# Performance work log

Hardware: AMD Instinct MI355X
Metric: run time of the kernel (lower is better)

## Reference

```python
import math
import jax, jax.numpy as jnp
import numpy as np

NUM_HEADS = 16
QUERY_SIZE = 1024
SEQ = 2048
HEAD = QUERY_SIZE // NUM_HEADS  # qk_size = vo_size = 64


def setup_inputs() -> dict:
    key = jax.random.key(0)
    ks = jax.random.split(key, 8)
    s = 0.02
    query = jax.random.normal(ks[0], (SEQ, QUERY_SIZE), jnp.float32)
    key_ = jax.random.normal(ks[1], (SEQ, QUERY_SIZE), jnp.float32)
    value = jax.random.normal(ks[2], (SEQ, QUERY_SIZE), jnp.float32)
    # causal mask (mask='causal' with state=None -> offset 0)
    mask = jnp.tril(jnp.ones((SEQ, SEQ), dtype=bool))
    Wq = jax.random.normal(ks[3], (QUERY_SIZE, QUERY_SIZE), jnp.float32) * s
    Wk = jax.random.normal(ks[4], (QUERY_SIZE, QUERY_SIZE), jnp.float32) * s
    Wv = jax.random.normal(ks[5], (QUERY_SIZE, QUERY_SIZE), jnp.float32) * s
    Wo = jax.random.normal(ks[6], (QUERY_SIZE, QUERY_SIZE), jnp.float32) * s
    return {"query": query, "key_": key_, "value": value, "mask": mask,
            "Wq": Wq, "Wk": Wk, "Wv": Wv, "Wo": Wo}


def reference(query, key_, value, mask, Wq, Wk, Wv, Wo):
    H, D = NUMS = NUM_HEADS, HEAD
    S = query.shape[0]
    inv_sqrt_d = 1.0 / math.sqrt(D)
    # per-token linear projections, split into heads: [S, H, D]
    q = (query @ Wq.T).reshape(S, H, D)
    k = (key_ @ Wk.T).reshape(S, H, D)
    v = (value @ Wv.T).reshape(S, H, D)
    # NOTE: original divides BOTH q and k by sqrt(d) (effective 1/d scaling)
    q = q * inv_sqrt_d
    k = k * inv_sqrt_d
    # logits per head: [H, S, S]
    logits = jnp.einsum('shd,Shd->hsS', q, k)
    logits = jnp.where(mask[None, :, :], logits, jnp.finfo(logits.dtype).min)
    # per-head GLOBAL max subtraction, softmax in fp32, cast back (faithful)
    m = jnp.max(logits, axis=(1, 2), keepdims=True)
    weights = jax.nn.softmax((logits - m).astype(jnp.float32), axis=-1).astype(query.dtype)
    attn = jnp.einsum('hsS,ShD->shD', weights, v).reshape(S, H * D)
    return attn @ Wo.T
```

## Files before the change

kernel.cpp:

```cpp
#include <hip/hip_runtime.h>
#include <hip/hip_bf16.h>

typedef __bf16 bf16_t;
typedef __bf16 bf16x8 __attribute__((ext_vector_type(8)));
typedef float f32x4 __attribute__((ext_vector_type(4)));

#define MFMA(A, B, C) __builtin_amdgcn_mfma_f32_16x16x32_bf16(A, B, C, 0, 0, 0)

#define GLL16(g, l) __builtin_amdgcn_global_load_lds(                      \
    (const __attribute__((address_space(1))) void*)(g),                    \
    (__attribute__((address_space(3))) void*)(l), 16, 0, 0)

__global__ __launch_bounds__(256) void cvt_all(
    const float* __restrict__ q, const float* __restrict__ k, const float* __restrict__ v,
    const float* __restrict__ wq, const float* __restrict__ wk,
    const float* __restrict__ wv, const float* __restrict__ wo,
    bf16_t* __restrict__ xq, bf16_t* __restrict__ xk, bf16_t* __restrict__ xv,
    bf16_t* __restrict__ ywq, bf16_t* __restrict__ ywk,
    bf16_t* __restrict__ ywv, bf16_t* __restrict__ ywo)
{
  const long gid = (long)blockIdx.x * 256 + threadIdx.x;
  const float* s; bf16_t* d; long off; float sc = 1.0f;
  if (gid < 262144)       { s = q;  d = xq;  off = gid; }
  else if (gid < 524288)  { s = k;  d = xk;  off = gid - 262144; }
  else if (gid < 786432)  { s = v;  d = xv;  off = gid - 524288; }
  else if (gid < 917504)  { s = wq; d = ywq; off = gid - 786432;  sc = 0.125f; }
  else if (gid < 1048576) { s = wk; d = ywk; off = gid - 917504;  sc = 0.125f; }
  else if (gid < 1179648) { s = wv; d = ywv; off = gid - 1048576; }
  else                    { s = wo; d = ywo; off = gid - 1179648; }
  const float* p = s + off * 8;
  float4 a = *(const float4*)p, b = *(const float4*)(p + 4);
  bf16x8 o;
  o[0] = (bf16_t)(a.x * sc); o[1] = (bf16_t)(a.y * sc);
  o[2] = (bf16_t)(a.z * sc); o[3] = (bf16_t)(a.w * sc);
  o[4] = (bf16_t)(b.x * sc); o[5] = (bf16_t)(b.y * sc);
  o[6] = (bf16_t)(b.z * sc); o[7] = (bf16_t)(b.w * sc);
  *(bf16x8*)(d + off * 8) = o;
}

__device__ __forceinline__ void gemm_core(const bf16_t* __restrict__ A,
                                          const bf16_t* __restrict__ W,
                                          int bm, int bn,
                                          bf16_t (&As)[2][128 * 64],
                                          bf16_t (&Bs)[2][64 * 64],
                                          f32x4 (&acc)[4][2])
{
  const int tid = threadIdx.x, lane = tid & 63, wave = tid >> 6;
  const int l15 = lane & 15, l4 = lane >> 4, l7 = l15 & 7;
  const int wm = (wave >> 1) * 64, wn = (wave & 1) * 32;

  auto stage = [&](int buf, int k0) {
#pragma unroll
    for (int i = 0; i < 4; ++i) {
      const int id = i * 256 + tid, row = id >> 3, cph = id & 7;
      GLL16(A + (size_t)(bm + row) * 1024 + k0 + 8 * (cph ^ (row & 7)),
            &As[buf][(i * 256 + wave * 64) * 8]);
    }
#pragma unroll
    for (int i = 0; i < 2; ++i) {
      const int id = i * 256 + tid, row = id >> 3, cph = id & 7;
      GLL16(W + (size_t)(bn + row) * 1024 + k0 + 8 * (cph ^ (row & 7)),
            &Bs[buf][(i * 256 + wave * 64) * 8]);
    }
  };

  stage(0, 0);
#pragma unroll
  for (int s = 0; s < 16; ++s) {
    if (s + 1 < 16) stage((s + 1) & 1, (s + 1) * 64);
    __syncthreads();
    const bf16_t* as = As[s & 1];
    const bf16_t* bs = Bs[s & 1];
#pragma unroll
    for (int ks = 0; ks < 2; ++ks) {
      bf16x8 af[4], bfr[2];
#pragma unroll
      for (int i = 0; i < 4; ++i)
        af[i] = *(const bf16x8*)(&as[(wm + i * 16 + l15) * 64 + 8 * ((ks * 4 + l4) ^ l7)]);
#pragma unroll
      for (int j = 0; j < 2; ++j)
        bfr[j] = *(const bf16x8*)(&bs[(wn + j * 16 + l15) * 64 + 8 * ((ks * 4 + l4) ^ l7)]);
#pragma unroll
      for (int i = 0; i < 4; ++i)
#pragma unroll
        for (int j = 0; j < 2; ++j)
          acc[i][j] = MFMA(af[i], bfr[j], acc[i][j]);
    }
    __syncthreads();
  }
}

__global__ __launch_bounds__(256) void gemm_qkv(
    const bf16_t* __restrict__ xq, const bf16_t* __restrict__ xk, const bf16_t* __restrict__ xv,
    const bf16_t* __restrict__ ywq, const bf16_t* __restrict__ ywk, const bf16_t* __restrict__ ywv,
    bf16_t* __restrict__ qo, bf16_t* __restrict__ ko, bf16_t* __restrict__ vt)
{
  __shared__ __align__(16) bf16_t As[2][128 * 64];
  __shared__ __align__(16) bf16_t Bs[2][64 * 64];
  const int z = blockIdx.z;
  const bf16_t* A = z == 0 ? xq : z == 1 ? xk : xv;
  const bf16_t* W = z == 0 ? ywq : z == 1 ? ywk : ywv;
  const int bm = blockIdx.x * 128, bn = blockIdx.y * 64;
  f32x4 acc[4][2] = {};
  gemm_core(A, W, bm, bn, As, Bs, acc);
  const int tid = threadIdx.x, lane = tid & 63, wave = tid >> 6;
  const int l15 = lane & 15, l4 = lane >> 4;
  const int wm = (wave >> 1) * 64, wn = (wave & 1) * 32;
  if (z < 2) {
    bf16_t* C = z == 0 ? qo : ko;
#pragma unroll
    for (int i = 0; i < 4; ++i)
#pragma unroll
      for (int j = 0; j < 2; ++j)
#pragma unroll
        for (int r = 0; r < 4; ++r)
          C[(size_t)(bm + wm + i * 16 + 4 * l4 + r) * 1024 + bn + wn + j * 16 + l15] =
              (bf16_t)acc[i][j][r];
  } else {
#pragma unroll
    for (int i = 0; i < 4; ++i)
#pragma unroll
      for (int j = 0; j < 2; ++j)
#pragma unroll
        for (int r = 0; r < 4; ++r)
          vt[(size_t)(bn + wn + j * 16 + l15) * 2048 + bm + wm + i * 16 + 4 * l4 + r] =
              (bf16_t)acc[i][j][r];
  }
}

__global__ __launch_bounds__(256) void gemm_out(
    const bf16_t* __restrict__ ctx, const bf16_t* __restrict__ ywo, float* __restrict__ out)
{
  __shared__ __align__(16) bf16_t As[2][128 * 64];
  __shared__ __align__(16) bf16_t Bs[2][64 * 64];
  const int bm = blockIdx.x * 128, bn = blockIdx.y * 64;
  f32x4 acc[4][2] = {};
  gemm_core(ctx, ywo, bm, bn, As, Bs, acc);
  const int tid = threadIdx.x, lane = tid & 63, wave = tid >> 6;
  const int l15 = lane & 15, l4 = lane >> 4;
  const int wm = (wave >> 1) * 64, wn = (wave & 1) * 32;
#pragma unroll
  for (int i = 0; i < 4; ++i)
#pragma unroll
    for (int j = 0; j < 2; ++j)
#pragma unroll
      for (int r = 0; r < 4; ++r)
        out[(size_t)(bm + wm + i * 16 + 4 * l4 + r) * 1024 + bn + wn + j * 16 + l15] =
            acc[i][j][r];
}

__global__ __launch_bounds__(1024) void attn1024(
    const bf16_t* __restrict__ Qb, const bf16_t* __restrict__ Kb,
    const bf16_t* __restrict__ Vt, bf16_t* __restrict__ Ctx)
{
  __shared__ __align__(16) char pool[64 * 1024 + 16 * 16 * 40 * 2 + 3 * 64 * 4];
  bf16_t* KsP = (bf16_t*)pool;
  bf16_t* VsP = (bf16_t*)(pool + 32 * 1024);
  bf16_t* PsP = (bf16_t*)(pool + 64 * 1024);
  float*  Osc = (float*)pool;
  float*  Dsc = (float*)(pool + 64 * 1024 + 16 * 16 * 40 * 2);

  const int bid = blockIdx.x;
  const int h = 2 * (bid & 7) + (bid >> 7);
  const int jp = (bid >> 3) & 15;
  const int hoff = h * 64;
  const int tid = threadIdx.x, lane = tid & 63, wave = tid >> 6;
  const int qg = wave & 3, kh = wave >> 2;
  const int l15 = lane & 15, l4 = lane >> 4, l7 = l15 & 7;

  const int qtA = jp, qtB = 31 - jp;
  const int qbA = qtA * 64, qbB = qtB * 64;
  const int nscB = qtB / 2 + 1;
  const int qmaxA = qbA + 16 * qg + 15;
  const int qmaxB = qbB + 16 * qg + 15;

  bf16x8 qA[2], qB[2];
#pragma unroll
  for (int kc = 0; kc < 2; ++kc) {
    qA[kc] = *(const bf16x8*)(Qb + (size_t)(qbA + 16 * qg + l15) * 1024 + hoff + 32 * kc + 8 * l4);
    qB[kc] = *(const bf16x8*)(Qb + (size_t)(qbB + 16 * qg + l15) * 1024 + hoff + 32 * kc + 8 * l4);
  }

  f32x4 oA[4] = {}, oB[4] = {};
  float dA[4] = {0.f, 0.f, 0.f, 0.f}, dB[4] = {0.f, 0.f, 0.f, 0.f};

  bf16x8 rk, rv;
  auto issue = [&](int sc) {
    const int t0 = sc * 128;
    const int kr = tid >> 3, kc = tid & 7;
    rk = *(const bf16x8*)(Kb + (size_t)(t0 + kr) * 1024 + hoff + 8 * kc);
    const int vr = tid >> 4, vc = tid & 15;
    rv = *(const bf16x8*)(Vt + (size_t)(hoff + vr) * 2048 + t0 + 8 * vc);
  };
  auto commit = [&](int buf) {
    const int kr = tid >> 3, kc = tid & 7;
    *(bf16x8*)(&KsP[buf * 8192 + kr * 64 + 8 * (kc ^ (kr & 7))]) = rk;
    const int vr = tid >> 4, vc = tid & 15;
    *(bf16x8*)(&VsP[buf * 8192 + vr * 128 + 8 * (vc ^ (vr & 7))]) = rv;
  };

  bf16_t* Pw = &PsP[wave * 640];
  auto PROC1 = [&](int cur, int sc, int qb, int qmax, const bf16x8 (&qf)[2],
                   f32x4 (&oacc)[4], float (&den)[4]) {
    const int tb = sc * 128 + kh * 32;
    if (tb > qmax) return;
    const bf16_t* Ksb = KsP + cur * 8192;
    const bf16_t* Vsb = VsP + cur * 8192;
    f32x4 sv[2] = {};
#pragma unroll
    for (int tf = 0; tf < 2; ++tf) {
      const int krow = 32 * kh + 16 * tf + l15;
      bf16x8 kf0 = *(const bf16x8*)(&Ksb[krow * 64 + 8 * (l4 ^ l7)]);
      bf16x8 kf1 = *(const bf16x8*)(&Ksb[krow * 64 + 8 * ((4 + l4) ^ l7)]);
      sv[tf] = MFMA(qf[0], kf0, sv[tf]);
      sv[tf] = MFMA(qf[1], kf1, sv[tf]);
    }
#pragma unroll
    for (int tf = 0; tf < 2; ++tf) {
      const int t = tb + 16 * tf + l15;
#pragma unroll
      for (int r = 0; r < 4; ++r) {
        const int qq = qb + 16 * qg + 4 * l4 + r;
        const float p = (t <= qq) ? __expf(sv[tf][r]) : 0.0f;
        const bf16_t pb = (bf16_t)p;
        den[r] += (float)pb;
        Pw[(4 * l4 + r) * 40 + 16 * tf + l15] = pb;
      }
    }
    asm volatile("s_waitcnt lgkmcnt(0)" ::: "memory");
    bf16x8 pa = *(const bf16x8*)(&Pw[l15 * 40 + 8 * l4]);
#pragma unroll
    for (int df = 0; df < 4; ++df) {
      const int vrow = 16 * df + l15;
      bf16x8 vf = *(const bf16x8*)(&Vsb[vrow * 128 + 8 * ((4 * kh + l4) ^ l7)]);
      oacc[df] = MFMA(pa, vf, oacc[df]);
    }
  };

  issue(0);
  commit(0);
  int cur = 0;
  for (int sc = 0; sc < nscB; ++sc) {
    const bool pre = (sc + 1 < nscB);
    if (pre) issue(sc + 1);
    __syncthreads();
    PROC1(cur, sc, qbB, qmaxB, qB, oB, dB);
    PROC1(cur, sc, qbA, qmaxA, qA, oA, dA);
    if (pre) commit(cur ^ 1);
    cur ^= 1;
  }

#pragma unroll
  for (int r = 0; r < 4; ++r)
#pragma unroll
    for (int m = 1; m < 16; m <<= 1) {
      dA[r] += __shfl_xor(dA[r], m, 64);
      dB[r] += __shfl_xor(dB[r], m, 64);
    }

  auto combine = [&](int qb, f32x4 (&oacc)[4], float (&den)[4]) {
    __syncthreads();
    if (kh > 0) {
      const int rl = qg * 16 + 4 * l4;
#pragma unroll
      for (int r = 0; r < 4; ++r) {
#pragma unroll
        for (int df = 0; df < 4; ++df)
          Osc[((kh - 1) * 64 + rl + r) * 66 + 16 * df + l15] = oacc[df][r];
        if (l15 == 0) Dsc[(kh - 1) * 64 + rl + r] = den[r];
      }
    }
    __syncthreads();
    if (kh == 0) {
#pragma unroll
      for (int r = 0; r < 4; ++r) {
        const int row = qg * 16 + 4 * l4 + r;
        const float dt = den[r] + Dsc[row] + Dsc[64 + row] + Dsc[128 + row];
        const float inv = 1.0f / dt;
#pragma unroll
        for (int df = 0; df < 4; ++df) {
          const int col = 16 * df + l15;
          const float s = oacc[df][r] + Osc[row * 66 + col] +
                          Osc[(64 + row) * 66 + col] + Osc[(128 + row) * 66 + col];
          Ctx[(size_t)(qb + row) * 1024 + hoff + col] = (bf16_t)(s * inv);
        }
      }
    }
  };
  combine(qbA, oA, dA);
  combine(qbB, oB, dB);
}

extern "C" void kernel_launch(void* const* d_in, const int* in_sizes, int n_in,
                              void* d_out, int out_size, void* d_ws, size_t ws_size,
                              hipStream_t stream)
{
  const float* query = (const float*)d_in[0];
  const float* key_  = (const float*)d_in[1];
  const float* value = (const float*)d_in[2];
  const float* Wq = (const float*)d_in[4];
  const float* Wk = (const float*)d_in[5];
  const float* Wv = (const float*)d_in[6];
  const float* Wo = (const float*)d_in[7];
  float* out = (float*)d_out;

  const size_t SE = (size_t)2048 * 1024, EE = (size_t)1024 * 1024;
  bf16_t* xq  = (bf16_t*)d_ws;
  bf16_t* xk  = xq + SE;
  bf16_t* xv  = xk + SE;
  bf16_t* wq  = xv + SE;
  bf16_t* wk  = wq + EE;
  bf16_t* wv  = wk + EE;
  bf16_t* wo  = wv + EE;
  bf16_t* qo  = wo + EE;
  bf16_t* ko  = qo + SE;
  bf16_t* vt  = ko + SE;
  bf16_t* ctx = vt + SE;

  cvt_all<<<5120, 256, 0, stream>>>(query, key_, value, Wq, Wk, Wv, Wo,
                                    xq, xk, xv, wq, wk, wv, wo);
  gemm_qkv<<<dim3(16, 16, 3), 256, 0, stream>>>(xq, xk, xv, wq, wk, wv, qo, ko, vt);
  attn1024<<<256, 1024, 0, stream>>>(qo, ko, vt, ctx);
  gemm_out<<<dim3(16, 16), 256, 0, stream>>>(ctx, wo, out);
}
```

Before: 71.54 us.

## Split attention into one 512-thread block per query tile with exp2 and mask specialization

Replaces the paired-tile 1024-thread attention kernel with a 512-thread kernel that handles one 64-row query tile per block, two key halves per 64-key chunk, launched heaviest tiles first across 512 blocks. Folds log2(e) into the Wk bf16 conversion so the softmax can use the hardware exp2 directly. Adds a compile-time unmasked path for chunks fully below the diagonal and accumulates the denominator from fp32 rather than rounded bf16 values. The aim is better occupancy and load balance and less per-element work, at the cost of more blocks and a denominator that no longer matches the bf16-rounded weights exactly.

Result: slower. 75.58 us (+5.6%).

```diff
diff --git a/kernel.cpp b/kernel.cpp
--- a/kernel.cpp
+++ b/kernel.cpp
@@ -25,7 +25,7 @@
   else if (gid < 524288)  { s = k;  d = xk;  off = gid - 262144; }
   else if (gid < 786432)  { s = v;  d = xv;  off = gid - 524288; }
   else if (gid < 917504)  { s = wq; d = ywq; off = gid - 786432;  sc = 0.125f; }
-  else if (gid < 1048576) { s = wk; d = ywk; off = gid - 917504;  sc = 0.125f; }
+  else if (gid < 1048576) { s = wk; d = ywk; off = gid - 917504;  sc = 0.125f * 1.44269504f; }
   else if (gid < 1179648) { s = wv; d = ywv; off = gid - 1048576; }
   else                    { s = wo; d = ywo; off = gid - 1179648; }
   const float* p = s + off * 8;
@@ -149,63 +149,56 @@
             acc[i][j][r];
 }
 
-__global__ __launch_bounds__(1024) void attn1024(
+__global__ __launch_bounds__(512) void attn512v2(
     const bf16_t* __restrict__ Qb, const bf16_t* __restrict__ Kb,
     const bf16_t* __restrict__ Vt, bf16_t* __restrict__ Ctx)
 {
-  __shared__ __align__(16) char pool[64 * 1024 + 16 * 16 * 40 * 2 + 3 * 64 * 4];
+  __shared__ __align__(16) char pool[16384 + 16384 + 10240 + 256];
   bf16_t* KsP = (bf16_t*)pool;
-  bf16_t* VsP = (bf16_t*)(pool + 32 * 1024);
-  bf16_t* PsP = (bf16_t*)(pool + 64 * 1024);
+  bf16_t* VsP = (bf16_t*)(pool + 16384);
+  bf16_t* PsP = (bf16_t*)(pool + 32768);
   float*  Osc = (float*)pool;
-  float*  Dsc = (float*)(pool + 64 * 1024 + 16 * 16 * 40 * 2);
+  float*  Dsc = (float*)(pool + 43008);
 
   const int bid = blockIdx.x;
-  const int h = 2 * (bid & 7) + (bid >> 7);
-  const int jp = (bid >> 3) & 15;
+  const int qt = 31 - (bid >> 4);
+  const int h = bid & 15;
   const int hoff = h * 64;
   const int tid = threadIdx.x, lane = tid & 63, wave = tid >> 6;
   const int qg = wave & 3, kh = wave >> 2;
   const int l15 = lane & 15, l4 = lane >> 4, l7 = l15 & 7;
 
-  const int qtA = jp, qtB = 31 - jp;
-  const int qbA = qtA * 64, qbB = qtB * 64;
-  const int nscB = qtB / 2 + 1;
-  const int qmaxA = qbA + 16 * qg + 15;
-  const int qmaxB = qbB + 16 * qg + 15;
-
-  bf16x8 qA[2], qB[2];
-#pragma unroll
-  for (int kc = 0; kc < 2; ++kc) {
-    qA[kc] = *(const bf16x8*)(Qb + (size_t)(qbA + 16 * qg + l15) * 1024 + hoff + 32 * kc + 8 * l4);
-    qB[kc] = *(const bf16x8*)(Qb + (size_t)(qbB + 16 * qg + l15) * 1024 + hoff + 32 * kc + 8 * l4);
-  }
-
-  f32x4 oA[4] = {}, oB[4] = {};
-  float dA[4] = {0.f, 0.f, 0.f, 0.f}, dB[4] = {0.f, 0.f, 0.f, 0.f};
+  const int qb = qt * 64;
+  const int nch = qt + 1;
+  const int qmin = qb + 16 * qg;
+
+  bf16x8 qf[2];
+#pragma unroll
+  for (int kc = 0; kc < 2; ++kc)
+    qf[kc] = *(const bf16x8*)(Qb + (size_t)(qb + 16 * qg + l15) * 1024 + hoff + 32 * kc + 8 * l4);
+
+  f32x4 oacc[4] = {};
+  float den[4] = {0.f, 0.f, 0.f, 0.f};
 
   bf16x8 rk, rv;
-  auto issue = [&](int sc) {
-    const int t0 = sc * 128;
+  auto issue = [&](int c) {
+    const int t0 = c * 64;
     const int kr = tid >> 3, kc = tid & 7;
     rk = *(const bf16x8*)(Kb + (size_t)(t0 + kr) * 1024 + hoff + 8 * kc);
-    const int vr = tid >> 4, vc = tid & 15;
-    rv = *(const bf16x8*)(Vt + (size_t)(hoff + vr) * 2048 + t0 + 8 * vc);
+    rv = *(const bf16x8*)(Vt + (size_t)(hoff + kr) * 2048 + t0 + 8 * kc);
   };
   auto commit = [&](int buf) {
     const int kr = tid >> 3, kc = tid & 7;
-    *(bf16x8*)(&KsP[buf * 8192 + kr * 64 + 8 * (kc ^ (kr & 7))]) = rk;
-    const int vr = tid >> 4, vc = tid & 15;
-    *(bf16x8*)(&VsP[buf * 8192 + vr * 128 + 8 * (vc ^ (vr & 7))]) = rv;
+    *(bf16x8*)(&KsP[buf * 4096 + kr * 64 + 8 * (kc ^ (kr & 7))]) = rk;
+    *(bf16x8*)(&VsP[buf * 4096 + kr * 64 + 8 * (kc ^ (kr & 7))]) = rv;
   };
 
   bf16_t* Pw = &PsP[wave * 640];
-  auto PROC1 = [&](int cur, int sc, int qb, int qmax, const bf16x8 (&qf)[2],
-                   f32x4 (&oacc)[4], float (&den)[4]) {
-    const int tb = sc * 128 + kh * 32;
-    if (tb > qmax) return;
-    const bf16_t* Ksb = KsP + cur * 8192;
-    const bf16_t* Vsb = VsP + cur * 8192;
+  auto PROC = [&](int cur, int c, auto masked) {
+    const int tb = c * 64 + kh * 32;
+    if (tb > qmin + 15) return;
+    const bf16_t* Ksb = KsP + cur * 4096;
+    const bf16_t* Vsb = VsP + cur * 4096;
     f32x4 sv[2] = {};
 #pragma unroll
     for (int tf = 0; tf < 2; ++tf) {
@@ -220,11 +213,13 @@
       const int t = tb + 16 * tf + l15;
 #pragma unroll
       for (int r = 0; r < 4; ++r) {
-        const int qq = qb + 16 * qg + 4 * l4 + r;
-        const float p = (t <= qq) ? __expf(sv[tf][r]) : 0.0f;
-        const bf16_t pb = (bf16_t)p;
-        den[r] += (float)pb;
-        Pw[(4 * l4 + r) * 40 + 16 * tf + l15] = pb;
+        float p = __builtin_amdgcn_exp2f(sv[tf][r]);
+        if constexpr (decltype(masked)::value) {
+          const int qq = qb + 16 * qg + 4 * l4 + r;
+          p = (t <= qq) ? p : 0.0f;
+        }
+        den[r] += p;
+        Pw[(4 * l4 + r) * 40 + 16 * tf + l15] = (bf16_t)p;
       }
     }
     asm volatile("s_waitcnt lgkmcnt(0)" ::: "memory");
@@ -232,7 +227,7 @@
 #pragma unroll
     for (int df = 0; df < 4; ++df) {
       const int vrow = 16 * df + l15;
-      bf16x8 vf = *(const bf16x8*)(&Vsb[vrow * 128 + 8 * ((4 * kh + l4) ^ l7)]);
+      bf16x8 vf = *(const bf16x8*)(&Vsb[vrow * 64 + 8 * ((4 * kh + l4) ^ l7)]);
       oacc[df] = MFMA(pa, vf, oacc[df]);
     }
   };
@@ -240,12 +235,15 @@
   issue(0);
   commit(0);
   int cur = 0;
-  for (int sc = 0; sc < nscB; ++sc) {
-    const bool pre = (sc + 1 < nscB);
-    if (pre) issue(sc + 1);
+  for (int c = 0; c < nch; ++c) {
+    const bool pre = (c + 1 < nch);
+    if (pre) issue(c + 1);
     __syncthreads();
-    PROC1(cur, sc, qbB, qmaxB, qB, oB, dB);
-    PROC1(cur, sc, qbA, qmaxA, qA, oA, dA);
+    const int tb = c * 64 + kh * 32;
+    if (tb + 31 <= qmin)
+      PROC(cur, c, std::integral_constant<bool, false>{});
+    else
+      PROC(cur, c, std::integral_constant<bool, true>{});
     if (pre) commit(cur ^ 1);
     cur ^= 1;
   }
@@ -253,42 +251,34 @@
 #pragma unroll
   for (int r = 0; r < 4; ++r)
 #pragma unroll
-    for (int m = 1; m < 16; m <<= 1) {
-      dA[r] += __shfl_xor(dA[r], m, 64);
-      dB[r] += __shfl_xor(dB[r], m, 64);
-    }
-
-  auto combine = [&](int qb, f32x4 (&oacc)[4], float (&den)[4]) {
-    __syncthreads();
-    if (kh > 0) {
-      const int rl = qg * 16 + 4 * l4;
-#pragma unroll
-      for (int r = 0; r < 4; ++r) {
-#pragma unroll
-        for (int df = 0; df < 4; ++df)
-          Osc[((kh - 1) * 64 + rl + r) * 66 + 16 * df + l15] = oacc[df][r];
-        if (l15 == 0) Dsc[(kh - 1) * 64 + rl + r] = den[r];
+    for (int m = 1; m < 16; m <<= 1)
+      den[r] += __shfl_xor(den[r], m, 64);
+
+  __syncthreads();
+  if (kh == 1) {
+    const int rl = qg * 16 + 4 * l4;
+#pragma unroll
+    for (int r = 0; r < 4; ++r) {
+#pragma unroll
+      for (int df = 0; df < 4; ++df)
+        Osc[(rl + r) * 66 + 16 * df + l15] = oacc[df][r];
+      if (l15 == 0) Dsc[rl + r] = den[r];
+    }
+  }
+  __syncthreads();
+  if (kh == 0) {
+#pragma unroll
+    for (int r = 0; r < 4; ++r) {
+      const int row = qg * 16 + 4 * l4 + r;
+      const float inv = 1.0f / (den[r] + Dsc[row]);
+#pragma unroll
+      for (int df = 0; df < 4; ++df) {
+        const int col = 16 * df + l15;
+        const float s = oacc[df][r] + Osc[row * 66 + col];
+        Ctx[(size_t)(qb + row) * 1024 + hoff + col] = (bf16_t)(s * inv);
       }
     }
-    __syncthreads();
-    if (kh == 0) {
-#pragma unroll
-      for (int r = 0; r < 4; ++r) {
-        const int row = qg * 16 + 4 * l4 + r;
-        const float dt = den[r] + Dsc[row] + Dsc[64 + row] + Dsc[128 + row];
-        const float inv = 1.0f / dt;
-#pragma unroll
-        for (int df = 0; df < 4; ++df) {
-          const int col = 16 * df + l15;
-          const float s = oacc[df][r] + Osc[row * 66 + col] +
-                          Osc[(64 + row) * 66 + col] + Osc[(128 + row) * 66 + col];
-          Ctx[(size_t)(qb + row) * 1024 + hoff + col] = (bf16_t)(s * inv);
-        }
-      }
-    }
-  };
-  combine(qbA, oA, dA);
-  combine(qbB, oB, dB);
+  }
 }
 
 extern "C" void kernel_launch(void* const* d_in, const int* in_sizes, int n_in,
@@ -320,6 +310,6 @@
   cvt_all<<<5120, 256, 0, stream>>>(query, key_, value, Wq, Wk, Wv, Wo,
                                     xq, xk, xv, wq, wk, wv, wo);
   gemm_qkv<<<dim3(16, 16, 3), 256, 0, stream>>>(xq, xk, xv, wq, wk, wv, qo, ko, vt);
-  attn1024<<<256, 1024, 0, stream>>>(qo, ko, vt, ctx);
+  attn512v2<<<512, 512, 0, stream>>>(qo, ko, vt, ctx);
   gemm_out<<<dim3(16, 16), 256, 0, stream>>>(ctx, wo, out);
 }
```

## Double KV chunk size, share K fragments across both query tiles, use exp2

Applied to the files above, without the earlier changes.

The K/V chunk staged per iteration grows from 128 to 256 keys, which halves the number of block barriers and doubles the LDS buffers. Processing of the two paired query tiles is merged, so each K fragment read from LDS feeds the MFMAs for both tiles. The log2(e) factor is folded into the Wk conversion scale so the softmax can use the hardware exp2 instruction instead of __expf. The cost is much more shared memory (about 148KB) and more registers, which could limit occupancy. The coarser chunks also do more masked work near the causal diagonal.

Measured after the change: 79.05 us. 10.5% more time.

```diff
diff --git a/kernel.cpp b/kernel.cpp
--- a/kernel.cpp
+++ b/kernel.cpp
@@ -25,7 +25,7 @@
   else if (gid < 524288)  { s = k;  d = xk;  off = gid - 262144; }
   else if (gid < 786432)  { s = v;  d = xv;  off = gid - 524288; }
   else if (gid < 917504)  { s = wq; d = ywq; off = gid - 786432;  sc = 0.125f; }
-  else if (gid < 1048576) { s = wk; d = ywk; off = gid - 917504;  sc = 0.125f; }
+  else if (gid < 1048576) { s = wk; d = ywk; off = gid - 917504;  sc = 0.125f * 1.44269504f; }
   else if (gid < 1179648) { s = wv; d = ywv; off = gid - 1048576; }
   else                    { s = wo; d = ywo; off = gid - 1179648; }
   const float* p = s + off * 8;
@@ -153,12 +153,12 @@
     const bf16_t* __restrict__ Qb, const bf16_t* __restrict__ Kb,
     const bf16_t* __restrict__ Vt, bf16_t* __restrict__ Ctx)
 {
-  __shared__ __align__(16) char pool[64 * 1024 + 16 * 16 * 40 * 2 + 3 * 64 * 4];
+  __shared__ __align__(16) char pool[64 * 1024 + 64 * 1024 + 16 * 640 * 2];
   bf16_t* KsP = (bf16_t*)pool;
-  bf16_t* VsP = (bf16_t*)(pool + 32 * 1024);
-  bf16_t* PsP = (bf16_t*)(pool + 64 * 1024);
+  bf16_t* VsP = (bf16_t*)(pool + 65536);
+  bf16_t* PsP = (bf16_t*)(pool + 131072);
   float*  Osc = (float*)pool;
-  float*  Dsc = (float*)(pool + 64 * 1024 + 16 * 16 * 40 * 2);
+  float*  Dsc = (float*)(pool + 50688);
 
   const int bid = blockIdx.x;
   const int h = 2 * (bid & 7) + (bid >> 7);
@@ -170,7 +170,7 @@
 
   const int qtA = jp, qtB = 31 - jp;
   const int qbA = qtA * 64, qbB = qtB * 64;
-  const int nscB = qtB / 2 + 1;
+  const int nscB = qtB / 4 + 1;
   const int qmaxA = qbA + 16 * qg + 15;
   const int qmaxB = qbB + 16 * qg + 15;
 
@@ -184,56 +184,95 @@
   f32x4 oA[4] = {}, oB[4] = {};
   float dA[4] = {0.f, 0.f, 0.f, 0.f}, dB[4] = {0.f, 0.f, 0.f, 0.f};
 
-  bf16x8 rk, rv;
+  bf16x8 rk[2], rv[2];
   auto issue = [&](int sc) {
-    const int t0 = sc * 128;
-    const int kr = tid >> 3, kc = tid & 7;
-    rk = *(const bf16x8*)(Kb + (size_t)(t0 + kr) * 1024 + hoff + 8 * kc);
-    const int vr = tid >> 4, vc = tid & 15;
-    rv = *(const bf16x8*)(Vt + (size_t)(hoff + vr) * 2048 + t0 + 8 * vc);
+    const int t0 = sc * 256;
+#pragma unroll
+    for (int i = 0; i < 2; ++i) {
+      const int id = tid + 1024 * i;
+      const int kr = id >> 3, kc = id & 7;
+      rk[i] = *(const bf16x8*)(Kb + (size_t)(t0 + kr) * 1024 + hoff + 8 * kc);
+      const int vr = id >> 5, vc = id & 31;
+      rv[i] = *(const bf16x8*)(Vt + (size_t)(hoff + vr) * 2048 + t0 + 8 * vc);
+    }
   };
   auto commit = [&](int buf) {
-    const int kr = tid >> 3, kc = tid & 7;
-    *(bf16x8*)(&KsP[buf * 8192 + kr * 64 + 8 * (kc ^ (kr & 7))]) = rk;
-    const int vr = tid >> 4, vc = tid & 15;
-    *(bf16x8*)(&VsP[buf * 8192 + vr * 128 + 8 * (vc ^ (vr & 7))]) = rv;
+#pragma unroll
+    for (int i = 0; i < 2; ++i) {
+      const int id = tid + 1024 * i;
+      const int kr = id >> 3, kc = id & 7;
+      *(bf16x8*)(&KsP[buf * 16384 + kr * 64 + 8 * (kc ^ (kr & 7))]) = rk[i];
+      const int vr = id >> 5, vc = id & 31;
+      *(bf16x8*)(&VsP[buf * 16384 + vr * 256 + 8 * (vc ^ (vr & 7))]) = rv[i];
+    }
   };
 
   bf16_t* Pw = &PsP[wave * 640];
-  auto PROC1 = [&](int cur, int sc, int qb, int qmax, const bf16x8 (&qf)[2],
-                   f32x4 (&oacc)[4], float (&den)[4]) {
-    const int tb = sc * 128 + kh * 32;
-    if (tb > qmax) return;
-    const bf16_t* Ksb = KsP + cur * 8192;
-    const bf16_t* Vsb = VsP + cur * 8192;
-    f32x4 sv[2] = {};
-#pragma unroll
-    for (int tf = 0; tf < 2; ++tf) {
-      const int krow = 32 * kh + 16 * tf + l15;
-      bf16x8 kf0 = *(const bf16x8*)(&Ksb[krow * 64 + 8 * (l4 ^ l7)]);
-      bf16x8 kf1 = *(const bf16x8*)(&Ksb[krow * 64 + 8 * ((4 + l4) ^ l7)]);
-      sv[tf] = MFMA(qf[0], kf0, sv[tf]);
-      sv[tf] = MFMA(qf[1], kf1, sv[tf]);
-    }
-#pragma unroll
-    for (int tf = 0; tf < 2; ++tf) {
-      const int t = tb + 16 * tf + l15;
-#pragma unroll
-      for (int r = 0; r < 4; ++r) {
-        const int qq = qb + 16 * qg + 4 * l4 + r;
-        const float p = (t <= qq) ? __expf(sv[tf][r]) : 0.0f;
-        const bf16_t pb = (bf16_t)p;
-        den[r] += (float)pb;
-        Pw[(4 * l4 + r) * 40 + 16 * tf + l15] = pb;
-      }
-    }
-    asm volatile("s_waitcnt lgkmcnt(0)" ::: "memory");
-    bf16x8 pa = *(const bf16x8*)(&Pw[l15 * 40 + 8 * l4]);
-#pragma unroll
-    for (int df = 0; df < 4; ++df) {
-      const int vrow = 16 * df + l15;
-      bf16x8 vf = *(const bf16x8*)(&Vsb[vrow * 128 + 8 * ((4 * kh + l4) ^ l7)]);
-      oacc[df] = MFMA(pa, vf, oacc[df]);
+  auto PROC = [&](int cur, int sc) {
+    const bf16_t* Ksb = KsP + cur * 16384;
+    const bf16_t* Vsb = VsP + cur * 16384;
+#pragma unroll
+    for (int half = 0; half < 2; ++half) {
+      const int tbh = sc * 256 + kh * 64 + 32 * half;
+      const bool doB = tbh <= qmaxB;
+      const bool doA = tbh <= qmaxA;
+      if (!doB) continue;
+      f32x4 svB[2] = {}, svA[2] = {};
+#pragma unroll
+      for (int tf = 0; tf < 2; ++tf) {
+        const int krow = 64 * kh + 32 * half + 16 * tf + l15;
+        bf16x8 kf0 = *(const bf16x8*)(&Ksb[krow * 64 + 8 * (l4 ^ l7)]);
+        bf16x8 kf1 = *(const bf16x8*)(&Ksb[krow * 64 + 8 * ((4 + l4) ^ l7)]);
+        svB[tf] = MFMA(qB[0], kf0, svB[tf]);
+        svB[tf] = MFMA(qB[1], kf1, svB[tf]);
+        if (doA) {
+          svA[tf] = MFMA(qA[0], kf0, svA[tf]);
+          svA[tf] = MFMA(qA[1], kf1, svA[tf]);
+        }
+      }
+      const int vbase = kh * 8 + half * 4 + l4;
+#pragma unroll
+      for (int tf = 0; tf < 2; ++tf) {
+        const int t = tbh + 16 * tf + l15;
+#pragma unroll
+        for (int r = 0; r < 4; ++r) {
+          const int qq = qbB + 16 * qg + 4 * l4 + r;
+          const float p = (t <= qq) ? __builtin_amdgcn_exp2f(svB[tf][r]) : 0.0f;
+          const bf16_t pb = (bf16_t)p;
+          dB[r] += (float)pb;
+          Pw[(4 * l4 + r) * 40 + 16 * tf + l15] = pb;
+        }
+      }
+      asm volatile("s_waitcnt lgkmcnt(0)" ::: "memory");
+      {
+        bf16x8 pa = *(const bf16x8*)(&Pw[l15 * 40 + 8 * l4]);
+#pragma unroll
+        for (int df = 0; df < 4; ++df) {
+          bf16x8 vf = *(const bf16x8*)(&VsP[cur * 16384 + (16 * df + l15) * 256 + 8 * (vbase ^ l7)]);
+          oB[df] = MFMA(pa, vf, oB[df]);
+        }
+      }
+      if (doA) {
+#pragma unroll
+        for (int tf = 0; tf < 2; ++tf) {
+          const int t = tbh + 16 * tf + l15;
+#pragma unroll
+          for (int r = 0; r < 4; ++r) {
+            const int qq = qbA + 16 * qg + 4 * l4 + r;
+            const float p = (t <= qq) ? __builtin_amdgcn_exp2f(svA[tf][r]) : 0.0f;
+            const bf16_t pb = (bf16_t)p;
+            dA[r] += (float)pb;
+            Pw[(4 * l4 + r) * 40 + 16 * tf + l15] = pb;
+          }
+        }
+        asm volatile("s_waitcnt lgkmcnt(0)" ::: "memory");
+        bf16x8 pa = *(const bf16x8*)(&Pw[l15 * 40 + 8 * l4]);
+#pragma unroll
+        for (int df = 0; df < 4; ++df) {
+          bf16x8 vf = *(const bf16x8*)(&Vsb[(16 * df + l15) * 256 + 8 * (vbase ^ l7)]);
+          oA[df] = MFMA(pa, vf, oA[df]);
+        }
+      }
     }
   };
 
@@ -244,8 +283,7 @@
     const bool pre = (sc + 1 < nscB);
     if (pre) issue(sc + 1);
     __syncthreads();
-    PROC1(cur, sc, qbB, qmaxB, qB, oB, dB);
-    PROC1(cur, sc, qbA, qmaxA, qA, oA, dA);
+    PROC(cur, sc);
     if (pre) commit(cur ^ 1);
     cur ^= 1;
   }
```

## Fuse fp32 weight conversion into GEMM B-tile loads and use exp2 with log2e folding

Applied to the files above, without the earlier changes.

Removes the separate weight-conversion pass. Each GEMM now loads fp32 weight tiles into registers, converts and scales them, and writes bf16 to LDS, software-pipelined one stage ahead. The log2(e) factor is folded into the Wk scale so attention can use the native exp2 instead of __expf. s_setprio is raised around the attention MFMA groups. The trade-off is that every GEMM block re-reads fp32 weights (twice the bytes of bf16) and spends VGPRs and ALU on the conversion, in exchange for skipping the weight conversion's write and re-read.

After: 79.71 us. +11.4%, slower.

```diff
diff --git a/kernel.cpp b/kernel.cpp
--- a/kernel.cpp
+++ b/kernel.cpp
@@ -11,35 +11,31 @@
     (const __attribute__((address_space(1))) void*)(g),                    \
     (__attribute__((address_space(3))) void*)(l), 16, 0, 0)
 
-__global__ __launch_bounds__(256) void cvt_all(
-    const float* __restrict__ q, const float* __restrict__ k, const float* __restrict__ v,
-    const float* __restrict__ wq, const float* __restrict__ wk,
-    const float* __restrict__ wv, const float* __restrict__ wo,
-    bf16_t* __restrict__ xq, bf16_t* __restrict__ xk, bf16_t* __restrict__ xv,
-    bf16_t* __restrict__ ywq, bf16_t* __restrict__ ywk,
-    bf16_t* __restrict__ ywv, bf16_t* __restrict__ ywo)
-{
-  const long gid = (long)blockIdx.x * 256 + threadIdx.x;
-  const float* s; bf16_t* d; long off; float sc = 1.0f;
-  if (gid < 262144)       { s = q;  d = xq;  off = gid; }
-  else if (gid < 524288)  { s = k;  d = xk;  off = gid - 262144; }
-  else if (gid < 786432)  { s = v;  d = xv;  off = gid - 524288; }
-  else if (gid < 917504)  { s = wq; d = ywq; off = gid - 786432;  sc = 0.125f; }
-  else if (gid < 1048576) { s = wk; d = ywk; off = gid - 917504;  sc = 0.125f; }
-  else if (gid < 1179648) { s = wv; d = ywv; off = gid - 1048576; }
-  else                    { s = wo; d = ywo; off = gid - 1179648; }
-  const float* p = s + off * 8;
-  float4 a = *(const float4*)p, b = *(const float4*)(p + 4);
+static __device__ __forceinline__ bf16x8 cvt8p(const float4& a, const float4& b, float sc) {
   bf16x8 o;
   o[0] = (bf16_t)(a.x * sc); o[1] = (bf16_t)(a.y * sc);
   o[2] = (bf16_t)(a.z * sc); o[3] = (bf16_t)(a.w * sc);
   o[4] = (bf16_t)(b.x * sc); o[5] = (bf16_t)(b.y * sc);
   o[6] = (bf16_t)(b.z * sc); o[7] = (bf16_t)(b.w * sc);
-  *(bf16x8*)(d + off * 8) = o;
+  return o;
+}
+
+__global__ __launch_bounds__(256) void cvt_act(
+    const float* __restrict__ q, const float* __restrict__ k, const float* __restrict__ v,
+    bf16_t* __restrict__ xq, bf16_t* __restrict__ xk, bf16_t* __restrict__ xv)
+{
+  const long gid = (long)blockIdx.x * 256 + threadIdx.x;
+  const float* s; bf16_t* d; long off;
+  if (gid < 262144)       { s = q; d = xq; off = gid; }
+  else if (gid < 524288)  { s = k; d = xk; off = gid - 262144; }
+  else                    { s = v; d = xv; off = gid - 524288; }
+  const float* p = s + off * 8;
+  float4 a = *(const float4*)p, b = *(const float4*)(p + 4);
+  *(bf16x8*)(d + off * 8) = cvt8p(a, b, 1.0f);
 }
 
 __device__ __forceinline__ void gemm_core(const bf16_t* __restrict__ A,
-                                          const bf16_t* __restrict__ W,
+                                          const float* __restrict__ W, float wsc,
                                           int bm, int bn,
                                           bf16_t (&As)[2][128 * 64],
                                           bf16_t (&Bs)[2][64 * 64],
@@ -49,26 +45,43 @@
   const int l15 = lane & 15, l4 = lane >> 4, l7 = l15 & 7;
   const int wm = (wave >> 1) * 64, wn = (wave & 1) * 32;
 
-  auto stage = [&](int buf, int k0) {
+  auto stageA = [&](int buf, int k0) {
 #pragma unroll
     for (int i = 0; i < 4; ++i) {
       const int id = i * 256 + tid, row = id >> 3, cph = id & 7;
       GLL16(A + (size_t)(bm + row) * 1024 + k0 + 8 * (cph ^ (row & 7)),
             &As[buf][(i * 256 + wave * 64) * 8]);
     }
+  };
+  float4 rw[2][2];
+  auto wload = [&](int k0) {
 #pragma unroll
     for (int i = 0; i < 2; ++i) {
-      const int id = i * 256 + tid, row = id >> 3, cph = id & 7;
-      GLL16(W + (size_t)(bn + row) * 1024 + k0 + 8 * (cph ^ (row & 7)),
-            &Bs[buf][(i * 256 + wave * 64) * 8]);
-    }
-  };
-
-  stage(0, 0);
+      const int id = i * 256 + tid, row = id >> 3, c = id & 7;
+      const float* p = W + (size_t)(bn + row) * 1024 + k0 + 8 * c;
+      rw[i][0] = *(const float4*)p; rw[i][1] = *(const float4*)(p + 4);
+    }
+  };
+  auto wcommit = [&](int buf) {
+#pragma unroll
+    for (int i = 0; i < 2; ++i) {
+      const int id = i * 256 + tid, row = id >> 3, c = id & 7;
+      *(bf16x8*)(&Bs[buf][row * 64 + 8 * (c ^ (row & 7))]) = cvt8p(rw[i][0], rw[i][1], wsc);
+    }
+  };
+
+  wload(0);
+  stageA(0, 0);
+  wcommit(0);
+  wload(64);
 #pragma unroll
   for (int s = 0; s < 16; ++s) {
-    if (s + 1 < 16) stage((s + 1) & 1, (s + 1) * 64);
-    __syncthreads();
+    if (s + 1 < 16) stageA((s + 1) & 1, (s + 1) * 64);
+    __syncthreads();
+    if (s + 1 < 16) {
+      wcommit((s + 1) & 1);
+      if (s + 2 < 16) wload((s + 2) * 64);
+    }
     const bf16_t* as = As[s & 1];
     const bf16_t* bs = Bs[s & 1];
 #pragma unroll
@@ -92,17 +105,18 @@
 
 __global__ __launch_bounds__(256) void gemm_qkv(
     const bf16_t* __restrict__ xq, const bf16_t* __restrict__ xk, const bf16_t* __restrict__ xv,
-    const bf16_t* __restrict__ ywq, const bf16_t* __restrict__ ywk, const bf16_t* __restrict__ ywv,
+    const float* __restrict__ Wq, const float* __restrict__ Wk, const float* __restrict__ Wv,
     bf16_t* __restrict__ qo, bf16_t* __restrict__ ko, bf16_t* __restrict__ vt)
 {
   __shared__ __align__(16) bf16_t As[2][128 * 64];
   __shared__ __align__(16) bf16_t Bs[2][64 * 64];
   const int z = blockIdx.z;
   const bf16_t* A = z == 0 ? xq : z == 1 ? xk : xv;
-  const bf16_t* W = z == 0 ? ywq : z == 1 ? ywk : ywv;
+  const float* W = z == 0 ? Wq : z == 1 ? Wk : Wv;
+  const float wsc = z == 0 ? 0.125f : z == 1 ? 0.125f * 1.44269504f : 1.0f;
   const int bm = blockIdx.x * 128, bn = blockIdx.y * 64;
   f32x4 acc[4][2] = {};
-  gemm_core(A, W, bm, bn, As, Bs, acc);
+  gemm_core(A, W, wsc, bm, bn, As, Bs, acc);
   const int tid = threadIdx.x, lane = tid & 63, wave = tid >> 6;
   const int l15 = lane & 15, l4 = lane >> 4;
   const int wm = (wave >> 1) * 64, wn = (wave & 1) * 32;
@@ -129,13 +143,13 @@
 }
 
 __global__ __launch_bounds__(256) void gemm_out(
-    const bf16_t* __restrict__ ctx, const bf16_t* __restrict__ ywo, float* __restrict__ out)
+    const bf16_t* __restrict__ ctx, const float* __restrict__ Wo, float* __restrict__ out)
 {
   __shared__ __align__(16) bf16_t As[2][128 * 64];
   __shared__ __align__(16) bf16_t Bs[2][64 * 64];
   const int bm = blockIdx.x * 128, bn = blockIdx.y * 64;
   f32x4 acc[4][2] = {};
-  gemm_core(ctx, ywo, bm, bn, As, Bs, acc);
+  gemm_core(ctx, Wo, 1.0f, bm, bn, As, Bs, acc);
   const int tid = threadIdx.x, lane = tid & 63, wave = tid >> 6;
   const int l15 = lane & 15, l4 = lane >> 4;
   const int wm = (wave >> 1) * 64, wn = (wave & 1) * 32;
@@ -212,8 +226,10 @@
       const int krow = 32 * kh + 16 * tf + l15;
       bf16x8 kf0 = *(const bf16x8*)(&Ksb[krow * 64 + 8 * (l4 ^ l7)]);
       bf16x8 kf1 = *(const bf16x8*)(&Ksb[krow * 64 + 8 * ((4 + l4) ^ l7)]);
+      __builtin_amdgcn_s_setprio(1);
       sv[tf] = MFMA(qf[0], kf0, sv[tf]);
       sv[tf] = MFMA(qf[1], kf1, sv[tf]);
+      __builtin_amdgcn_s_setprio(0);
     }
 #pragma unroll
     for (int tf = 0; tf < 2; ++tf) {
@@ -221,7 +237,7 @@
 #pragma unroll
       for (int r = 0; r < 4; ++r) {
         const int qq = qb + 16 * qg + 4 * l4 + r;
-        const float p = (t <= qq) ? __expf(sv[tf][r]) : 0.0f;
+        const float p = (t <= qq) ? __builtin_amdgcn_exp2f(sv[tf][r]) : 0.0f;
         const bf16_t pb = (bf16_t)p;
         den[r] += (float)pb;
         Pw[(4 * l4 + r) * 40 + 16 * tf + l15] = pb;
@@ -229,12 +245,14 @@
     }
     asm volatile("s_waitcnt lgkmcnt(0)" ::: "memory");
     bf16x8 pa = *(const bf16x8*)(&Pw[l15 * 40 + 8 * l4]);
+    __builtin_amdgcn_s_setprio(1);
 #pragma unroll
     for (int df = 0; df < 4; ++df) {
       const int vrow = 16 * df + l15;
       bf16x8 vf = *(const bf16x8*)(&Vsb[vrow * 128 + 8 * ((4 * kh + l4) ^ l7)]);
       oacc[df] = MFMA(pa, vf, oacc[df]);
     }
+    __builtin_amdgcn_s_setprio(0);
   };
 
   issue(0);
@@ -304,22 +322,17 @@
   const float* Wo = (const float*)d_in[7];
   float* out = (float*)d_out;
 
-  const size_t SE = (size_t)2048 * 1024, EE = (size_t)1024 * 1024;
+  const size_t SE = (size_t)2048 * 1024;
   bf16_t* xq  = (bf16_t*)d_ws;
   bf16_t* xk  = xq + SE;
   bf16_t* xv  = xk + SE;
-  bf16_t* wq  = xv + SE;
-  bf16_t* wk  = wq + EE;
-  bf16_t* wv  = wk + EE;
-  bf16_t* wo  = wv + EE;
-  bf16_t* qo  = wo + EE;
+  bf16_t* qo  = xv + SE;
   bf16_t* ko  = qo + SE;
   bf16_t* vt  = ko + SE;
   bf16_t* ctx = vt + SE;
 
-  cvt_all<<<5120, 256, 0, stream>>>(query, key_, value, Wq, Wk, Wv, Wo,
-                                    xq, xk, xv, wq, wk, wv, wo);
-  gemm_qkv<<<dim3(16, 16, 3), 256, 0, stream>>>(xq, xk, xv, wq, wk, wv, qo, ko, vt);
+  cvt_act<<<3072, 256, 0, stream>>>(query, key_, value, xq, xk, xv);
+  gemm_qkv<<<dim3(16, 16, 3), 256, 0, stream>>>(xq, xk, xv, Wq, Wk, Wv, qo, ko, vt);
   attn1024<<<256, 1024, 0, stream>>>(qo, ko, vt, ctx);
-  gemm_out<<<dim3(16, 16), 256, 0, stream>>>(ctx, wo, out);
-}
+  gemm_out<<<dim3(16, 16), 256, 0, stream>>>(ctx, Wo, out);
+}
```
